# Kernel tuning notes

Hardware: AMD Instinct MI355X
Metric: run time of the kernel (lower is better)

The kernel has to match this reference:

```python
import jax, jax.numpy as jnp
import numpy as np

B, D_IN, L = 16, 16, 4096
H, N2, NL = 256, 32, 4


def setup_inputs() -> dict:
    key = jax.random.key(0)
    ks = jax.random.split(key, 16)
    log_dt = jnp.log(0.001) + jax.random.uniform(ks[3], (NL, H)) * (jnp.log(0.1) - jnp.log(0.001))
    return {
        "x": jax.random.normal(ks[0], (B, D_IN, L), jnp.float32),
        "enc_w": jax.random.normal(ks[1], (D_IN, H), jnp.float32) / np.sqrt(D_IN),
        "enc_b": jax.random.normal(ks[2], (H,), jnp.float32) * 0.01,
        "log_dt": log_dt.astype(jnp.float32),
        "A_re": jax.random.normal(ks[4], (NL, H, N2), jnp.float32) * 0.5,
        "A_im": jax.random.normal(ks[5], (NL, H, N2), jnp.float32) * np.pi,
        "C_re": jax.random.normal(ks[6], (NL, H, N2), jnp.float32),
        "C_im": jax.random.normal(ks[7], (NL, H, N2), jnp.float32),
        "D": jax.random.normal(ks[8], (NL, H), jnp.float32),
        "W_out": jax.random.normal(ks[9], (NL, H, H), jnp.float32) / np.sqrt(H),
        "b_out": jax.random.normal(ks[10], (NL, H), jnp.float32) * 0.01,
        "ln_w": jnp.ones((NL, H), jnp.float32),
        "ln_b": jnp.zeros((NL, H), jnp.float32),
        "dec_w": jax.random.normal(ks[11], (H, D_IN), jnp.float32) / np.sqrt(H),
        "dec_b": jax.random.normal(ks[12], (D_IN,), jnp.float32) * 0.01,
    }


def _s4_layer(z, log_dt, A_re, A_im, C_re, C_im, D, W_out, b_out):
    # z: (B, H, L). Diagonal SSM (S4D) with ZOH discretization + FFT causal conv.
    Ltot = z.shape[-1]
    dt = jnp.exp(log_dt)                              # (H,)
    A = -jnp.exp(A_re) + 1j * A_im                    # (H, N2) complex, Re<0
    C = C_re + 1j * C_im                              # (H, N2)
    dtA = A * dt[:, None]                             # (H, N2)
    Cc = C * (jnp.exp(dtA) - 1.0) / A                 # discretized C*B coefficients
    # Vandermonde: K[h,l] = 2*Re(sum_n Cc[h,n] * exp(dtA[h,n]*l))
    t = jnp.arange(Ltot)
    vand = jnp.exp(dtA[:, :, None] * t)               # (H, N2, L) complex
    K = 2.0 * jnp.einsum('hn,hnl->hl', Cc, vand).real # (H, L)
    nfft = 2 * Ltot
    y = jnp.fft.irfft(jnp.fft.rfft(z, n=nfft) * jnp.fft.rfft(K, n=nfft)[None], n=nfft)[..., :Ltot]
    y = y + z * D[None, :, None]                      # skip term
    y = jax.nn.gelu(y)                                # final_act='gelu'
    y = jnp.einsum('bhl,hd->bdl', y, W_out) + b_out[None, :, None]  # pointwise output linear
    return y


def _layernorm(x_bhl, w, b):
    # LayerNorm over channel dim H of (B, H, L)
    mu = jnp.mean(x_bhl, axis=1, keepdims=True)
    var = jnp.var(x_bhl, axis=1, keepdims=True)
    xn = (x_bhl - mu) * jax.lax.rsqrt(var + 1e-5)
    return xn * w[None, :, None] + b[None, :, None]


def reference(x, enc_w, enc_b, log_dt, A_re, A_im, C_re, C_im, D, W_out, b_out, ln_w, ln_b, dec_w, dec_b):
    # encoder: (B, d_in, L) -> (B, H, L)
    h = jnp.einsum('bil,ih->bhl', x, enc_w) + enc_b[None, :, None]
    for i in range(NL):
        z = _s4_layer(h, log_dt[i], A_re[i], A_im[i], C_re[i], C_im[i], D[i], W_out[i], b_out[i])
        h = z + h
        h = _layernorm(h, ln_w[i], ln_b[i])  # post-norm (prenorm=False)
    out = jnp.einsum('bhl,hd->bdl', h, dec_w) + dec_b[None, :, None]
    return out
```

## Files before the change

### kernel.cpp

```cpp
#include <hip/hip_runtime.h>
#include <hip/hip_bf16.h>
#include <math.h>

#define Bb 16
#define DIN 16
#define LL 4096
#define HH 256
#define NN2 32
#define NLAY 4
#define HN (HH*NN2)
#define BN 32

typedef __attribute__((ext_vector_type(8))) short short8;
typedef __attribute__((ext_vector_type(4))) short short4v;
typedef __attribute__((ext_vector_type(4))) float f32x4;
typedef unsigned short u16;

__device__ inline u16 f2bf(float f) {
  unsigned int x = __float_as_uint(f);
  unsigned int r = x + 0x7FFFu + ((x >> 16) & 1u);
  return (u16)(r >> 16);
}
__device__ inline float bf2f(u16 u) {
  return __uint_as_float(((unsigned int)u) << 16);
}
__device__ inline unsigned int packsplit(float v) {
  u16 hi = f2bf(v);
  u16 lo = f2bf(v - bf2f(hi));
  return (((unsigned int)hi) << 16) | lo;
}
__device__ inline unsigned int cvtpk(float a, float b) {
  unsigned int r;
  asm("v_cvt_pk_bf16_f32 %0, %1, %2" : "=v"(r) : "v"(a), "v"(b));
  return r;
}
__device__ inline short8 ld8(const u16* p) {
  short4v a = *(const short4v*)p;
  short4v b = *(const short4v*)(p + 16);
  return __builtin_shufflevector(a, b, 0, 1, 2, 3, 4, 5, 6, 7);
}
__device__ inline size_t fidx(int h, int m, int row, int col) {
  int wv = row >> 4, row16 = row & 15;
  int kh = col >> 5, c5 = col & 31;
  int lane = ((c5 & 15) >> 2) * 16 + row16;
  int j = (((c5 >> 4) & 1) << 2) | (c5 & 3);
  return ((((((size_t)h * 6 + m) * 4 + wv) * 2 + kh) * 64 + lane) << 3) + j;
}

__global__ __launch_bounds__(256) void enc_kernel(const float* __restrict__ x,
    const float* __restrict__ ew, const float* __restrict__ eb,
    float* __restrict__ hbuf) {
  int blk = blockIdx.x;
  int tile = blk & 15;
  int h = (blk >> 4) & (HH - 1);
  int b = blk >> 12;
  int l = tile * 256 + threadIdx.x;
  const float* xb = x + (size_t)b * DIN * LL + l;
  float acc = eb[h];
  #pragma unroll
  for (int i = 0; i < DIN; ++i)
    acc = fmaf(xb[(size_t)i * LL], ew[i * HH + h], acc);
  hbuf[((size_t)(b * HH + h)) * LL + l] = acc;
}

__global__ __launch_bounds__(256) void basis_kernel(
    const float* __restrict__ log_dt, const float* __restrict__ Are,
    const float* __restrict__ Aim, const float* __restrict__ Cre,
    const float* __restrict__ Cim, float* __restrict__ w64,
    u16* __restrict__ Bf) {
  __shared__ float K_l[64];
  int h = blockIdx.x;
  int t = threadIdx.x;
  if (t < 32) {
    int n = t;
    int idx = h * 32 + n;
    float dt = expf(log_dt[h]);
    float ar = -expf(Are[idx]);
    float ai = Aim[idx];
    float er = expf(ar * dt);
    float wr = er * cosf(ai * dt);
    float wi = er * sinf(ai * dt);
    float nr = wr - 1.f, ni = wi;
    float inv = 1.f / (ar * ar + ai * ai);
    float qr = (nr * ar + ni * ai) * inv;
    float qi = (ni * ar - nr * ai) * inv;
    float crv = Cre[idx], civ = Cim[idx];
    float cr = 2.f * (crv * qr - civ * qi);
    float ci = 2.f * (crv * qi + civ * qr);
    float pr = wr, pi = wi;
    #pragma unroll
    for (int q = 0; q < 6; ++q) {
      float t0 = pr * pr - pi * pi;
      pi = 2.f * pr * pi;
      pr = t0;
    }
    w64[idx] = pr;
    w64[HN + idx] = pi;
    float vr = 1.f, vi = 0.f;
    for (int m = 0; m <= 64; ++m) {
      float e = cr * vr - ci * vi;
      float f = -(cr * vi + ci * vr);
      float s = e;
      s += __shfl_xor(s, 1); s += __shfl_xor(s, 2); s += __shfl_xor(s, 4);
      s += __shfl_xor(s, 8); s += __shfl_xor(s, 16);
      if (m <= 63) {
        if (n == 0) K_l[m] = s;
        int i = 63 - m;
        u16 hr = f2bf(vr);
        Bf[fidx(h, 2, 2 * n, i)] = hr;
        Bf[fidx(h, 3, 2 * n, i)] = f2bf(vr - bf2f(hr));
        u16 hi2 = f2bf(vi);
        Bf[fidx(h, 2, 2 * n + 1, i)] = hi2;
        Bf[fidx(h, 3, 2 * n + 1, i)] = f2bf(vi - bf2f(hi2));
      }
      if (m >= 1) {
        int row = m - 1;
        u16 he = f2bf(e);
        Bf[fidx(h, 4, row, 2 * n)] = he;
        Bf[fidx(h, 5, row, 2 * n)] = f2bf(e - bf2f(he));
        u16 hf = f2bf(f);
        Bf[fidx(h, 4, row, 2 * n + 1)] = hf;
        Bf[fidx(h, 5, row, 2 * n + 1)] = f2bf(f - bf2f(hf));
      }
      float nvr = vr * wr - vi * wi;
      float nvi = vr * wi + vi * wr;
      vr = nvr; vi = nvi;
    }
  }
  __syncthreads();
  #pragma unroll
  for (int p = 0; p < 16; ++p) {
    int id = p * 256 + t;
    int j = id >> 6, i = id & 63;
    float kv = (j >= i) ? K_l[j - i] : 0.f;
    u16 hi = f2bf(kv);
    Bf[fidx(h, 0, j, i)] = hi;
    Bf[fidx(h, 1, j, i)] = f2bf(kv - bf2f(hi));
  }
}

__global__ __launch_bounds__(256) void wpack_kernel(const float* __restrict__ W,
                                                    unsigned int* __restrict__ Wp) {
  int idx = blockIdx.x * 256 + threadIdx.x;
  int j = idx & 7;
  int lane = (idx >> 3) & 63;
  int di = (idx >> 9) & 3;
  int ks = (idx >> 11) & 7;
  int wv = idx >> 14;
  int row16 = lane & 15, kgrp = lane >> 4;
  int d = wv * 64 + di * 16 + row16;
  int hcol = ks * 32 + kgrp * 4 + (j & 3) + ((j >> 2) << 4);
  Wp[idx] = packsplit(W[hcol * HH + d]);
}

__global__ __launch_bounds__(256, 4) void s4_mfma_kernel(
    const float* __restrict__ zg, const float* __restrict__ w64,
    const float* __restrict__ Dvec, const u16* __restrict__ Bf,
    unsigned int* __restrict__ gout) {
  __shared__ u16 zh[64 * 68], zl[64 * 68];
  __shared__ float stT[64 * 68];
  u16* sh = (u16*)stT;
  u16* sl = sh + 64 * 68;
  unsigned int* packbuf = (unsigned int*)stT;
  int bh = blockIdx.x, h = bh & (HH - 1), t = threadIdx.x;
  int wv = t >> 6, lane = t & 63, row16 = lane & 15, kgrp = lane >> 4;
  const u16* BfH = Bf + (size_t)h * (6 * 4 * 2 * 64 * 8);
  #define LDF(m, kh) (*(const short8*)(BfH + (((m) * 4 + wv) * 2 + (kh)) * 512 + lane * 8))
  short8 fTh0 = LDF(0, 0), fTh1 = LDF(0, 1);
  short8 fTl0 = LDF(1, 0), fTl1 = LDF(1, 1);
  short8 fMh0 = LDF(2, 0), fMh1 = LDF(2, 1);
  short8 fMl0 = LDF(3, 0), fMl1 = LDF(3, 1);
  const float* zrow = zg + (size_t)bh * LL;
  int c0 = t >> 2, i0 = (t & 3) * 16;
  {
    const float4* zsrc = (const float4*)(zrow + c0 * 64 + i0);
    #pragma unroll
    for (int q = 0; q < 4; ++q) {
      float4 v = zsrc[q];
      unsigned int hp0 = cvtpk(v.x, v.y);
      unsigned int hp1 = cvtpk(v.z, v.w);
      float r0 = v.x - __uint_as_float(hp0 << 16);
      float r1 = v.y - __uint_as_float(hp0 & 0xFFFF0000u);
      float r2 = v.z - __uint_as_float(hp1 << 16);
      float r3 = v.w - __uint_as_float(hp1 & 0xFFFF0000u);
      unsigned int lp0 = cvtpk(r0, r1);
      unsigned int lp1 = cvtpk(r2, r3);
      int base = c0 * 68 + i0 + q * 4;
      *(unsigned int*)&zh[base] = hp0;
      *(unsigned int*)&zh[base + 2] = hp1;
      *(unsigned int*)&zl[base] = lp0;
      *(unsigned int*)&zl[base + 2] = lp1;
    }
  }
  __syncthreads();
  f32x4 y[4];
  #pragma unroll
  for (int ct = 0; ct < 4; ++ct) {
    f32x4 aS = (f32x4){0.f, 0.f, 0.f, 0.f};
    f32x4 aY = (f32x4){0.f, 0.f, 0.f, 0.f};
    int cc = ct * 16 + row16;
    #pragma unroll
    for (int kh = 0; kh < 2; ++kh) {
      int kb = kh * 32 + kgrp * 4;
      short8 Bh = ld8(&zh[cc * 68 + kb]);
      short8 Bl = ld8(&zl[cc * 68 + kb]);
      short8 Ah = kh ? fMh1 : fMh0;
      short8 Al = kh ? fMl1 : fMl0;
      aS = __builtin_amdgcn_mfma_f32_16x16x32_bf16(Ah, Bh, aS, 0, 0, 0);
      aS = __builtin_amdgcn_mfma_f32_16x16x32_bf16(Ah, Bl, aS, 0, 0, 0);
      aS = __builtin_amdgcn_mfma_f32_16x16x32_bf16(Al, Bh, aS, 0, 0, 0);
      short8 Ch = kh ? fTh1 : fTh0;
      short8 Cl = kh ? fTl1 : fTl0;
      aY = __builtin_amdgcn_mfma_f32_16x16x32_bf16(Ch, Bh, aY, 0, 0, 0);
      aY = __builtin_amdgcn_mfma_f32_16x16x32_bf16(Ch, Bl, aY, 0, 0, 0);
      aY = __builtin_amdgcn_mfma_f32_16x16x32_bf16(Cl, Bh, aY, 0, 0, 0);
    }
    y[ct] = aY;
    #pragma unroll
    for (int r = 0; r < 4; ++r)
      stT[(wv * 16 + kgrp * 4 + r) * 68 + cc] = aS[r];
  }
  __syncthreads();
  short8 fEh0 = LDF(4, 0), fEh1 = LDF(4, 1);
  short8 fEl0 = LDF(5, 0), fEl1 = LDF(5, 1);
  #undef LDF
  float ir[8], ii[8];
  {
    float xr[8], xi[8], pr[8], pi[8];
    #pragma unroll
    for (int k = 0; k < 8; ++k) {
      int d0 = wv * 16 + 2 * k;
      xr[k] = stT[d0 * 68 + lane];
      xi[k] = stT[(d0 + 1) * 68 + lane];
      pr[k] = w64[h * 32 + wv * 8 + k];
      pi[k] = w64[HN + h * 32 + wv * 8 + k];
    }
    #pragma unroll
    for (int d = 1; d < 64; d <<= 1) {
      #pragma unroll
      for (int k = 0; k < 8; ++k) {
        float qr = __shfl_up(xr[k], d);
        float qi = __shfl_up(xi[k], d);
        if (lane >= d) {
          xr[k] = fmaf(pr[k], qr, fmaf(-pi[k], qi, xr[k]));
          xi[k] = fmaf(pr[k], qi, fmaf(pi[k], qr, xi[k]));
        }
        float t0 = pr[k] * pr[k] - pi[k] * pi[k];
        pi[k] = 2.f * pr[k] * pi[k];
        pr[k] = t0;
      }
    }
    #pragma unroll
    for (int k = 0; k < 8; ++k) {
      ir[k] = __shfl_up(xr[k], 1);
      ii[k] = __shfl_up(xi[k], 1);
      if (lane == 0) { ir[k] = 0.f; ii[k] = 0.f; }
    }
  }
  __syncthreads();
  #pragma unroll
  for (int k = 0; k < 8; ++k) {
    int d0 = wv * 16 + 2 * k;
    unsigned int hp = cvtpk(ir[k], ii[k]);
    float rr = ir[k] - __uint_as_float(hp << 16);
    float ri = ii[k] - __uint_as_float(hp & 0xFFFF0000u);
    unsigned int lp = cvtpk(rr, ri);
    *(unsigned int*)&sh[lane * 68 + d0] = hp;
    *(unsigned int*)&sl[lane * 68 + d0] = lp;
  }
  __syncthreads();
  #pragma unroll
  for (int ct = 0; ct < 4; ++ct) {
    f32x4 a = y[ct];
    int cc = ct * 16 + row16;
    #pragma unroll
    for (int kh = 0; kh < 2; ++kh) {
      int kb = kh * 32 + kgrp * 4;
      short8 Sh8 = ld8(&sh[cc * 68 + kb]);
      short8 Sl8 = ld8(&sl[cc * 68 + kb]);
      short8 Ah = kh ? fEh1 : fEh0;
      short8 Al = kh ? fEl1 : fEl0;
      a = __builtin_amdgcn_mfma_f32_16x16x32_bf16(Ah, Sh8, a, 0, 0, 0);
      a = __builtin_amdgcn_mfma_f32_16x16x32_bf16(Ah, Sl8, a, 0, 0, 0);
      a = __builtin_amdgcn_mfma_f32_16x16x32_bf16(Al, Sh8, a, 0, 0, 0);
    }
    y[ct] = a;
  }
  __syncthreads();
  {
    float Dh = Dvec[h];
    int j0 = wv * 16 + kgrp * 4;
    #pragma unroll
    for (int ct = 0; ct < 4; ++ct) {
      int cc = ct * 16 + row16;
      unsigned int za = *(const unsigned int*)&zh[cc * 68 + j0];
      unsigned int zb = *(const unsigned int*)&zh[cc * 68 + j0 + 2];
      unsigned int la = *(const unsigned int*)&zl[cc * 68 + j0];
      unsigned int lb = *(const unsigned int*)&zl[cc * 68 + j0 + 2];
      float zf[4];
      zf[0] = __uint_as_float(za << 16) + __uint_as_float(la << 16);
      zf[1] = __uint_as_float(za & 0xFFFF0000u) + __uint_as_float(la & 0xFFFF0000u);
      zf[2] = __uint_as_float(zb << 16) + __uint_as_float(lb << 16);
      zf[3] = __uint_as_float(zb & 0xFFFF0000u) + __uint_as_float(lb & 0xFFFF0000u);
      float v[4];
      #pragma unroll
      for (int r = 0; r < 4; ++r) {
        float vv = fmaf(zf[r], Dh, y[ct][r]);
        float u = 1.5957691216057308f * fmaf(0.044715f * vv, vv * vv, vv);
        v[r] = vv / (1.f + __expf(-u));
      }
      unsigned int h01 = cvtpk(v[0], v[1]);
      unsigned int h23 = cvtpk(v[2], v[3]);
      float r0 = v[0] - __uint_as_float(h01 << 16);
      float r1 = v[1] - __uint_as_float(h01 & 0xFFFF0000u);
      float r2 = v[2] - __uint_as_float(h23 << 16);
      float r3 = v[3] - __uint_as_float(h23 & 0xFFFF0000u);
      unsigned int l01 = cvtpk(r0, r1);
      unsigned int l23 = cvtpk(r2, r3);
      uint4 w;
      w.x = (h01 << 16) | (l01 & 0xFFFFu);
      w.y = (h01 & 0xFFFF0000u) | (l01 >> 16);
      w.z = (h23 << 16) | (l23 & 0xFFFFu);
      w.w = (h23 & 0xFFFF0000u) | (l23 >> 16);
      *(uint4*)&packbuf[cc * 68 + j0] = w;
    }
  }
  __syncthreads();
  {
    unsigned int* grow = gout + (size_t)bh * LL;
    #pragma unroll
    for (int q = 0; q < 4; ++q) {
      uint4 v = *(const uint4*)&packbuf[c0 * 68 + i0 + q * 4];
      *(uint4*)&grow[c0 * 64 + i0 + q * 4] = v;
    }
  }
}

template<int LAST>
__global__ __launch_bounds__(256, 4) void mm_mfma_ln_kernel(
    const unsigned int* __restrict__ gp, float* __restrict__ h_buf,
    const unsigned int* __restrict__ Wp, const float* __restrict__ bo,
    const float* __restrict__ lw, const float* __restrict__ lb,
    const float* __restrict__ dcw, const float* __restrict__ dcb,
    float* __restrict__ outp) {
  __shared__ float smem[HH * 33];
  __shared__ float red_s[4][BN];
  __shared__ float red_q[4][BN];
  unsigned int* gt = (unsigned int*)smem;
  float* rt = smem;
  int blk = blockIdx.x;
  int b = blk >> 7;
  int l0 = (blk & 127) * BN;
  int t = threadIdx.x;
  const unsigned int* gbase = gp + (size_t)b * HH * LL + l0;
  #pragma unroll
  for (int p = 0; p < 4; ++p) {
    int hh = p * 64 + (t >> 2);
    int lq = (t & 3) * 8;
    const uint4* src = (const uint4*)(gbase + (size_t)hh * LL + lq);
    uint4 v0 = src[0];
    uint4 v1 = src[1];
    unsigned int vals[8] = {v0.x, v0.y, v0.z, v0.w, v1.x, v1.y, v1.z, v1.w};
    #pragma unroll
    for (int j = 0; j < 8; ++j) {
      int l = lq + j;
      int xm = (l & 7) ^ ((l >> 3) & 3);
      int g4 = (hh >> 2) ^ xm;
      gt[l * HH + g4 * 4 + (hh & 3)] = vals[j];
    }
  }
  __syncthreads();
  int wv = t >> 6, lane = t & 63;
  int row16 = lane & 15, kgrp = lane >> 4;
  f32x4 acc[4][2];
  #pragma unroll
  for (int di = 0; di < 4; ++di)
    #pragma unroll
    for (int li = 0; li < 2; ++li)
      acc[di][li] = (f32x4){0.f, 0.f, 0.f, 0.f};
  #pragma unroll 2
  for (int ks = 0; ks < 8; ++ks) {
    int h0 = ks * 32;
    short8 Bhi[2], Blo[2];
    #pragma unroll
    for (int li = 0; li < 2; ++li) {
      int l = li * 16 + row16;
      int xm = (l & 7) ^ ((l >> 3) & 3);
      int g4a = ((h0 >> 2) + kgrp) ^ xm;
      int g4b = ((h0 >> 2) + kgrp + 4) ^ xm;
      uint4 pa = *(const uint4*)&gt[l * HH + g4a * 4];
      uint4 pb = *(const uint4*)&gt[l * HH + g4b * 4];
      union { int i[4]; short8 s; } uh, ul;
      uh.i[0] = (int)((pa.x >> 16) | (pa.y & 0xFFFF0000u));
      uh.i[1] = (int)((pa.z >> 16) | (pa.w & 0xFFFF0000u));
      uh.i[2] = (int)((pb.x >> 16) | (pb.y & 0xFFFF0000u));
      uh.i[3] = (int)((pb.z >> 16) | (pb.w & 0xFFFF0000u));
      ul.i[0] = (int)((pa.x & 0xFFFFu) | (pa.y << 16));
      ul.i[1] = (int)((pa.z & 0xFFFFu) | (pa.w << 16));
      ul.i[2] = (int)((pb.x & 0xFFFFu) | (pb.y << 16));
      ul.i[3] = (int)((pb.z & 0xFFFFu) | (pb.w << 16));
      Bhi[li] = uh.s; Blo[li] = ul.s;
    }
    #pragma unroll
    for (int di = 0; di < 4; ++di) {
      const uint4* wf = (const uint4*)Wp + ((((wv * 8 + ks) * 4 + di) * 64 + lane) * 2);
      uint4 pa = wf[0];
      uint4 pb = wf[1];
      union { int i[4]; short8 s; } uh, ul;
      uh.i[0] = (int)((pa.x >> 16) | (pa.y & 0xFFFF0000u));
      uh.i[1] = (int)((pa.z >> 16) | (pa.w & 0xFFFF0000u));
      uh.i[2] = (int)((pb.x >> 16) | (pb.y & 0xFFFF0000u));
      uh.i[3] = (int)((pb.z >> 16) | (pb.w & 0xFFFF0000u));
      ul.i[0] = (int)((pa.x & 0xFFFFu) | (pa.y << 16));
      ul.i[1] = (int)((pa.z & 0xFFFFu) | (pa.w << 16));
      ul.i[2] = (int)((pb.x & 0xFFFFu) | (pb.y << 16));
      ul.i[3] = (int)((pb.z & 0xFFFFu) | (pb.w << 16));
      short8 Ahi = uh.s, Alo = ul.s;
      #pragma unroll
      for (int li = 0; li < 2; ++li) {
        acc[di][li] = __builtin_amdgcn_mfma_f32_16x16x32_bf16(Ahi, Bhi[li], acc[di][li], 0, 0, 0);
        acc[di][li] = __builtin_amdgcn_mfma_f32_16x16x32_bf16(Ahi, Blo[li], acc[di][li], 0, 0, 0);
        acc[di][li] = __builtin_amdgcn_mfma_f32_16x16x32_bf16(Alo, Bhi[li], acc[di][li], 0, 0, 0);
      }
    }
  }
  const float* hb = h_buf + (size_t)b * HH * LL + l0;
  #pragma unroll
  for (int di = 0; di < 4; ++di) {
    #pragma unroll
    for (int r = 0; r < 4; ++r) {
      int d = wv * 64 + di * 16 + kgrp * 4 + r;
      float bov = bo[d];
      #pragma unroll
      for (int li = 0; li < 2; ++li) {
        int l = li * 16 + row16;
        acc[di][li][r] += bov + hb[(size_t)d * LL + l];
      }
    }
  }
  #pragma unroll
  for (int li = 0; li < 2; ++li) {
    float s = 0.f, q = 0.f;
    #pragma unroll
    for (int di = 0; di < 4; ++di)
      #pragma unroll
      for (int r = 0; r < 4; ++r) {
        float v = acc[di][li][r];
        s += v;
        q = fmaf(v, v, q);
      }
    s += __shfl_xor(s, 16); s += __shfl_xor(s, 32);
    q += __shfl_xor(q, 16); q += __shfl_xor(q, 32);
    if (lane < 16) {
      red_s[wv][li * 16 + lane] = s;
      red_q[wv][li * 16 + lane] = q;
    }
  }
  __syncthreads();
  float mu[2], rstd[2];
  #pragma unroll
  for (int li = 0; li < 2; ++li) {
    int cl = li * 16 + row16;
    float s = red_s[0][cl] + red_s[1][cl] + red_s[2][cl] + red_s[3][cl];
    float q = red_q[0][cl] + red_q[1][cl] + red_q[2][cl] + red_q[3][cl];
    float m = s * (1.f / 256.f);
    float var = q * (1.f / 256.f) - m * m;
    mu[li] = m;
    rstd[li] = rsqrtf(var + 1e-5f);
  }
  if (!LAST) {
    float* hw = h_buf + (size_t)b * HH * LL + l0;
    #pragma unroll
    for (int di = 0; di < 4; ++di) {
      #pragma unroll
      for (int r = 0; r < 4; ++r) {
        int d = wv * 64 + di * 16 + kgrp * 4 + r;
        float lwv = lw[d], lbv = lb[d];
        #pragma unroll
        for (int li = 0; li < 2; ++li) {
          int l = li * 16 + row16;
          hw[(size_t)d * LL + l] = (acc[di][li][r] - mu[li]) * rstd[li] * lwv + lbv;
        }
      }
    }
  } else {
    #pragma unroll
    for (int di = 0; di < 4; ++di) {
      #pragma unroll
      for (int r = 0; r < 4; ++r) {
        int d = wv * 64 + di * 16 + kgrp * 4 + r;
        float lwv = lw[d], lbv = lb[d];
        #pragma unroll
        for (int li = 0; li < 2; ++li) {
          int l = li * 16 + row16;
          rt[d * 33 + l] = (acc[di][li][r] - mu[li]) * rstd[li] * lwv + lbv;
        }
      }
    }
    __syncthreads();
    int l = t & 31, dd = t >> 5;
    float a0 = dcb[dd], a1 = dcb[dd + 8];
    #pragma unroll 8
    for (int d = 0; d < HH; ++d) {
      float hv = rt[d * 33 + l];
      a0 = fmaf(hv, dcw[d * DIN + dd], a0);
      a1 = fmaf(hv, dcw[d * DIN + dd + 8], a1);
    }
    float* ob = outp + (size_t)b * DIN * LL + l0;
    ob[(size_t)dd * LL + l] = a0;
    ob[(size_t)(dd + 8) * LL + l] = a1;
  }
}

extern "C" void kernel_launch(void* const* d_in, const int* in_sizes, int n_in,
                              void* d_out, int out_size, void* d_ws, size_t ws_size,
                              hipStream_t stream) {
  const float* x      = (const float*)d_in[0];
  const float* enc_w  = (const float*)d_in[1];
  const float* enc_b  = (const float*)d_in[2];
  const float* log_dt = (const float*)d_in[3];
  const float* A_re   = (const float*)d_in[4];
  const float* A_im   = (const float*)d_in[5];
  const float* C_re   = (const float*)d_in[6];
  const float* C_im   = (const float*)d_in[7];
  const float* Dv     = (const float*)d_in[8];
  const float* W_out  = (const float*)d_in[9];
  const float* b_out  = (const float*)d_in[10];
  const float* ln_w   = (const float*)d_in[11];
  const float* ln_b   = (const float*)d_in[12];
  const float* dec_w  = (const float*)d_in[13];
  const float* dec_b  = (const float*)d_in[14];
  float* out = (float*)d_out;

  float* h_buf = (float*)d_ws;
  unsigned int* g_pack = (unsigned int*)(h_buf + (size_t)Bb * HH * LL);
  float* w64 = (float*)(g_pack + (size_t)Bb * HH * LL);
  unsigned int* Wp = (unsigned int*)(w64 + 2 * HN);
  u16* Bf = (u16*)(Wp + HH * HH);

  enc_kernel<<<Bb * HH * (LL / 256), 256, 0, stream>>>(x, enc_w, enc_b, h_buf);
  for (int i = 0; i < NLAY; ++i) {
    basis_kernel<<<HH, 256, 0, stream>>>(log_dt + i * HH, A_re + i * HN,
                                         A_im + i * HN, C_re + i * HN,
                                         C_im + i * HN, w64, Bf);
    wpack_kernel<<<HH * HH / 256, 256, 0, stream>>>(W_out + (size_t)i * HH * HH, Wp);
    s4_mfma_kernel<<<Bb * HH, 256, 0, stream>>>(h_buf, w64, Dv + i * HH, Bf, g_pack);
    if (i < NLAY - 1) {
      mm_mfma_ln_kernel<0><<<Bb * (LL / BN), 256, 0, stream>>>(
          g_pack, h_buf, Wp, b_out + i * HH, ln_w + i * HH, ln_b + i * HH,
          dec_w, dec_b, out);
    } else {
      mm_mfma_ln_kernel<1><<<Bb * (LL / BN), 256, 0, stream>>>(
          g_pack, h_buf, Wp, b_out + i * HH, ln_w + i * HH, ln_b + i * HH,
          dec_w, dec_b, out);
    }
  }
}
```

Measured before the change: 641.9 us.

## Shrink LDS footprint, prefetch W fragments, use v_perm for bf16 split unpack

```diff
diff --git a/kernel.cpp b/kernel.cpp
--- a/kernel.cpp
+++ b/kernel.cpp
@@ -38,6 +38,13 @@
   short4v a = *(const short4v*)p;
   short4v b = *(const short4v*)(p + 16);
   return __builtin_shufflevector(a, b, 0, 1, 2, 3, 4, 5, 6, 7);
+}
+#define PSEL_HI 0x07060302u
+#define PSEL_LO 0x05040100u
+__device__ inline short8 mk8(unsigned a, unsigned b, unsigned c, unsigned d) {
+  union { unsigned u[4]; short8 s; } r;
+  r.u[0] = a; r.u[1] = b; r.u[2] = c; r.u[3] = d;
+  return r.s;
 }
 __device__ inline size_t fidx(int h, int m, int row, int col) {
   int wv = row >> 4, row16 = row & 15;
@@ -337,17 +344,17 @@
 }
 
 template<int LAST>
-__global__ __launch_bounds__(256, 4) void mm_mfma_ln_kernel(
+__global__ __launch_bounds__(256, 5) void mm_mfma_ln_kernel(
     const unsigned int* __restrict__ gp, float* __restrict__ h_buf,
     const unsigned int* __restrict__ Wp, const float* __restrict__ bo,
     const float* __restrict__ lw, const float* __restrict__ lb,
     const float* __restrict__ dcw, const float* __restrict__ dcb,
     float* __restrict__ outp) {
-  __shared__ float smem[HH * 33];
-  __shared__ float red_s[4][BN];
-  __shared__ float red_q[4][BN];
-  unsigned int* gt = (unsigned int*)smem;
-  float* rt = smem;
+  __shared__ __align__(16) unsigned int smem[BN * HH];
+  unsigned int* gt = smem;
+  float* red_s = (float*)smem;
+  float* red_q = (float*)smem + 4 * BN;
+  float* rt = (float*)smem;
   int blk = blockIdx.x;
   int b = blk >> 7;
   int l0 = (blk & 127) * BN;
@@ -378,7 +385,14 @@
     #pragma unroll
     for (int li = 0; li < 2; ++li)
       acc[di][li] = (f32x4){0.f, 0.f, 0.f, 0.f};
-  #pragma unroll 2
+  uint4 wpa[4], wpb[4];
+  #pragma unroll
+  for (int di = 0; di < 4; ++di) {
+    const uint4* wf = (const uint4*)Wp + ((((wv * 8 + 0) * 4 + di) * 64 + lane) * 2);
+    wpa[di] = wf[0];
+    wpb[di] = wf[1];
+  }
+  #pragma unroll
   for (int ks = 0; ks < 8; ++ks) {
     int h0 = ks * 32;
     short8 Bhi[2], Blo[2];
@@ -390,32 +404,38 @@
       int g4b = ((h0 >> 2) + kgrp + 4) ^ xm;
       uint4 pa = *(const uint4*)&gt[l * HH + g4a * 4];
       uint4 pb = *(const uint4*)&gt[l * HH + g4b * 4];
-      union { int i[4]; short8 s; } uh, ul;
-      uh.i[0] = (int)((pa.x >> 16) | (pa.y & 0xFFFF0000u));
-      uh.i[1] = (int)((pa.z >> 16) | (pa.w & 0xFFFF0000u));
-      uh.i[2] = (int)((pb.x >> 16) | (pb.y & 0xFFFF0000u));
-      uh.i[3] = (int)((pb.z >> 16) | (pb.w & 0xFFFF0000u));
-      ul.i[0] = (int)((pa.x & 0xFFFFu) | (pa.y << 16));
-      ul.i[1] = (int)((pa.z & 0xFFFFu) | (pa.w << 16));
-      ul.i[2] = (int)((pb.x & 0xFFFFu) | (pb.y << 16));
-      ul.i[3] = (int)((pb.z & 0xFFFFu) | (pb.w << 16));
-      Bhi[li] = uh.s; Blo[li] = ul.s;
+      Bhi[li] = mk8(__builtin_amdgcn_perm(pa.y, pa.x, PSEL_HI),
+                    __builtin_amdgcn_perm(pa.w, pa.z, PSEL_HI),
+                    __builtin_amdgcn_perm(pb.y, pb.x, PSEL_HI),
+                    __builtin_amdgcn_perm(pb.w, pb.z, PSEL_HI));
+      Blo[li] = mk8(__builtin_amdgcn_perm(pa.y, pa.x, PSEL_LO),
+                    __builtin_amdgcn_perm(pa.w, pa.z, PSEL_LO),
+                    __builtin_amdgcn_perm(pb.y, pb.x, PSEL_LO),
+                    __builtin_amdgcn_perm(pb.w, pb.z, PSEL_LO));
+    }
+    uint4 cpa[4], cpb[4];
+    #pragma unroll
+    for (int di = 0; di < 4; ++di) { cpa[di] = wpa[di]; cpb[di] = wpb[di]; }
+    if (ks < 7) {
+      #pragma unroll
+      for (int di = 0; di < 4; ++di) {
+        const uint4* wf = (const uint4*)Wp + ((((wv * 8 + ks + 1) * 4 + di) * 64 + lane) * 2);
+        wpa[di] = wf[0];
+        wpb[di] = wf[1];
+      }
     }
     #pragma unroll
     for (int di = 0; di < 4; ++di) {
-      const uint4* wf = (const uint4*)Wp + ((((wv * 8 + ks) * 4 + di) * 64 + lane) * 2);
-      uint4 pa = wf[0];
-      uint4 pb = wf[1];
-      union { int i[4]; short8 s; } uh, ul;
-      uh.i[0] = (int)((pa.x >> 16) | (pa.y & 0xFFFF0000u));
-      uh.i[1] = (int)((pa.z >> 16) | (pa.w & 0xFFFF0000u));
-      uh.i[2] = (int)((pb.x >> 16) | (pb.y & 0xFFFF0000u));
-      uh.i[3] = (int)((pb.z >> 16) | (pb.w & 0xFFFF0000u));
-      ul.i[0] = (int)((pa.x & 0xFFFFu) | (pa.y << 16));
-      ul.i[1] = (int)((pa.z & 0xFFFFu) | (pa.w << 16));
-      ul.i[2] = (int)((pb.x & 0xFFFFu) | (pb.y << 16));
-      ul.i[3] = (int)((pb.z & 0xFFFFu) | (pb.w << 16));
-      short8 Ahi = uh.s, Alo = ul.s;
+      uint4 pa = cpa[di];
+      uint4 pb = cpb[di];
+      short8 Ahi = mk8(__builtin_amdgcn_perm(pa.y, pa.x, PSEL_HI),
+                       __builtin_amdgcn_perm(pa.w, pa.z, PSEL_HI),
+                       __builtin_amdgcn_perm(pb.y, pb.x, PSEL_HI),
+                       __builtin_amdgcn_perm(pb.w, pb.z, PSEL_HI));
+      short8 Alo = mk8(__builtin_amdgcn_perm(pa.y, pa.x, PSEL_LO),
+                       __builtin_amdgcn_perm(pa.w, pa.z, PSEL_LO),
+                       __builtin_amdgcn_perm(pb.y, pb.x, PSEL_LO),
+                       __builtin_amdgcn_perm(pb.w, pb.z, PSEL_LO));
       #pragma unroll
       for (int li = 0; li < 2; ++li) {
         acc[di][li] = __builtin_amdgcn_mfma_f32_16x16x32_bf16(Ahi, Bhi[li], acc[di][li], 0, 0, 0);
@@ -438,6 +458,7 @@
       }
     }
   }
+  __syncthreads();
   #pragma unroll
   for (int li = 0; li < 2; ++li) {
     float s = 0.f, q = 0.f;
@@ -452,8 +473,8 @@
     s += __shfl_xor(s, 16); s += __shfl_xor(s, 32);
     q += __shfl_xor(q, 16); q += __shfl_xor(q, 32);
     if (lane < 16) {
-      red_s[wv][li * 16 + lane] = s;
-      red_q[wv][li * 16 + lane] = q;
+      red_s[wv * BN + li * 16 + lane] = s;
+      red_q[wv * BN + li * 16 + lane] = q;
     }
   }
   __syncthreads();
@@ -461,8 +482,8 @@
   #pragma unroll
   for (int li = 0; li < 2; ++li) {
     int cl = li * 16 + row16;
-    float s = red_s[0][cl] + red_s[1][cl] + red_s[2][cl] + red_s[3][cl];
-    float q = red_q[0][cl] + red_q[1][cl] + red_q[2][cl] + red_q[3][cl];
+    float s = red_s[0 * BN + cl] + red_s[1 * BN + cl] + red_s[2 * BN + cl] + red_s[3 * BN + cl];
+    float q = red_q[0 * BN + cl] + red_q[1 * BN + cl] + red_q[2 * BN + cl] + red_q[3 * BN + cl];
     float m = s * (1.f / 256.f);
     float var = q * (1.f / 256.f) - m * m;
     mu[li] = m;
@@ -484,6 +505,7 @@
       }
     }
   } else {
+    __syncthreads();
     #pragma unroll
     for (int di = 0; di < 4; ++di) {
       #pragma unroll
@@ -493,7 +515,7 @@
         #pragma unroll
         for (int li = 0; li < 2; ++li) {
           int l = li * 16 + row16;
-          rt[d * 33 + l] = (acc[di][li][r] - mu[li]) * rstd[li] * lwv + lbv;
+          rt[d * BN + l] = (acc[di][li][r] - mu[li]) * rstd[li] * lwv + lbv;
         }
       }
     }
@@ -502,7 +524,7 @@
     float a0 = dcb[dd], a1 = dcb[dd + 8];
     #pragma unroll 8
     for (int d = 0; d < HH; ++d) {
-      float hv = rt[d * 33 + l];
+      float hv = rt[d * BN + l];
       a0 = fmaf(hv, dcw[d * DIN + dd], a0);
       a1 = fmaf(hv, dcw[d * DIN + dd + 8], a1);
     }
```

Result: slower. 661.8 us (+3.1%).
